# Optimization experiments

Measured on AMD Instinct MI355X. Metric: run time of the kernel, lower is better.

## Reference

```python
import jax, jax.numpy as jnp
import numpy as np

CLASSES = 21
IOU_THRESH = 0.5
ALPHA = 0.25   # focal loss alpha
GAMMA = 2.0    # focal loss gamma
SL1_BETA = 1.0 # torch SmoothL1Loss default beta
CLS_W = 1.0
REG_W = 1.0
NUM_ANCHORS = 98304
NUM_TARGETS = 1024


def _compute_iou(boxes_a, boxes_b):
    # boxes_a: [T,4], boxes_b: [A,4] in (x1,y1,x2,y2) -> [T,A]
    lt = jnp.maximum(boxes_a[:, None, :2], boxes_b[None, :, :2])
    rb = jnp.minimum(boxes_a[:, None, 2:], boxes_b[None, :, 2:])
    wh = jnp.clip(rb - lt, 0.0)
    inter = wh[..., 0] * wh[..., 1]
    area_a = (boxes_a[:, 2] - boxes_a[:, 0]) * (boxes_a[:, 3] - boxes_a[:, 1])
    area_b = (boxes_b[:, 2] - boxes_b[:, 0]) * (boxes_b[:, 3] - boxes_b[:, 1])
    union = area_a[:, None] + area_b[None, :] - inter
    return inter / jnp.maximum(union, 1e-8)


def _encode(boxes, anchors):
    bw = boxes[:, 2] - boxes[:, 0]
    bh = boxes[:, 3] - boxes[:, 1]
    bcx = boxes[:, 0] + 0.5 * bw
    bcy = boxes[:, 1] + 0.5 * bh
    aw = anchors[:, 2] - anchors[:, 0]
    ah = anchors[:, 3] - anchors[:, 1]
    acx = anchors[:, 0] + 0.5 * aw
    acy = anchors[:, 1] + 0.5 * ah
    tx = (bcx - acx) / aw
    ty = (bcy - acy) / ah
    tw = jnp.log(jnp.maximum(bw, 1e-8) / aw)
    th = jnp.log(jnp.maximum(bh, 1e-8) / ah)
    return jnp.stack([tx, ty, tw, th], axis=1)


def _focal_loss(logits, targets):
    # elementwise sigmoid focal loss (no reduction)
    p = jax.nn.sigmoid(logits)
    # numerically stable BCE with logits
    ce = jnp.maximum(logits, 0.0) - logits * targets + jnp.log1p(jnp.exp(-jnp.abs(logits)))
    p_t = p * targets + (1.0 - p) * (1.0 - targets)
    alpha_t = ALPHA * targets + (1.0 - ALPHA) * (1.0 - targets)
    return alpha_t * (1.0 - p_t) ** GAMMA * ce


def _smooth_l1(diff):
    ad = jnp.abs(diff)
    return jnp.where(ad < SL1_BETA, 0.5 * diff * diff / SL1_BETA, ad - 0.5 * SL1_BETA)


def setup_inputs() -> dict:
    key = jax.random.key(0)
    kA, kW, kT, kJ, kL, kC, kB = jax.random.split(key, 7)
    A, T = NUM_ANCHORS, NUM_TARGETS
    centers = jax.random.uniform(kA, (A, 2), minval=0.15, maxval=0.85)
    sizes = jax.random.uniform(kW, (A, 2), minval=0.05, maxval=0.30)
    anchors = jnp.concatenate([centers - 0.5 * sizes, centers + 0.5 * sizes], axis=1)
    # targets = jittered anchors so IoU >= 0.5 matches exist
    idx = jax.random.randint(kT, (T,), 0, A)
    jitter = jax.random.uniform(kJ, (T, 4), minval=-0.01, maxval=0.01)
    target_boxes = anchors[idx] + jitter
    target_labels = jax.random.randint(kL, (T,), 0, CLASSES)
    classification_preds = jax.random.normal(kC, (A, CLASSES), dtype=jnp.float32)
    boxes_preds = jax.random.normal(kB, (A, 4), dtype=jnp.float32)
    return {
        'classification_preds': classification_preds,
        'boxes_preds': boxes_preds,
        'anchors': anchors,
        'target_boxes': target_boxes,
        'target_labels': target_labels,
    }


def reference(classification_preds, boxes_preds, anchors, target_boxes, target_labels):
    iou = _compute_iou(target_boxes, anchors)  # [T, A]

    # anchor-side matching -> classification targets
    max_iou_for_anchors = jnp.max(iou, axis=0)          # [A]
    target_ids_for_anchors = jnp.argmax(iou, axis=0)     # [A]
    positive_mask = max_iou_for_anchors >= IOU_THRESH    # [A] bool
    n_pos = jnp.sum(positive_mask.astype(jnp.float32))
    onehot = jax.nn.one_hot(target_labels[target_ids_for_anchors], CLASSES, dtype=jnp.float32)
    cls_targets = jnp.where(positive_mask[:, None], onehot, 0.0)
    cls_loss = jnp.sum(_focal_loss(classification_preds, cls_targets)) / n_pos

    max_iou_for_targets = jnp.max(iou, axis=1)          # [T]
    anchor_ids_for_targets = jnp.argmax(iou, axis=1)     # [T]
    t_mask = (max_iou_for_targets >= IOU_THRESH).astype(jnp.float32)  # [T]
    matched_anchors = anchors[anchor_ids_for_targets]    # [T,4]
    encoded = _encode(target_boxes, matched_anchors)     # [T,4]
    pred = boxes_preds[anchor_ids_for_targets]           # [T,4]
    diff = (pred - encoded) * t_mask[:, None]
    n_match = jnp.maximum(jnp.sum(t_mask), 1.0)
    reg_loss = jnp.sum(_smooth_l1(diff)) / (n_match * 4.0)  # mean over matched elements

    w_cls = cls_loss * CLS_W
    w_reg = reg_loss * REG_W
    return (w_cls + w_reg, w_cls, w_reg)
```

## Files before the change

### kernel.cpp

```cpp
#include <hip/hip_runtime.h>
#include <stdint.h>

#define NA 98304
#define NT 1024
#define NC 21
#define ACH 96
#define TCH 16
#define NBLK (ACH * TCH)
#define HI_MIN 0xBF000000u


__device__ __forceinline__ float f0(float x) {
    const float ax = fabsf(x);
    const float u  = __expf(-ax);
    const float ce = fmaxf(x, 0.f) + __logf(1.f + u);
    const float p  = (x >= 0.f ? 1.f : u) / (1.f + u);
    return 0.75f * p * p * ce;
}
__device__ __forceinline__ float f1(float x) {
    const float ax = fabsf(x);
    const float u  = __expf(-ax);
    const float ce = fmaxf(x, 0.f) - x + __logf(1.f + u);
    const float p  = (x >= 0.f ? 1.f : u) / (1.f + u);
    const float q  = 1.f - p;
    return 0.25f * q * q * ce;
}
__device__ __forceinline__ unsigned long long mk_key(float iou, unsigned int idx) {
    return ((unsigned long long)(__float_as_uint(iou) | 0x80000000u) << 32) |
           (unsigned long long)(0xFFFFFFFFu - idx);
}
__device__ __forceinline__ float smooth_l1(float d) {
    const float ad = fabsf(d);
    return (ad < 1.f) ? 0.5f * d * d : ad - 0.5f;
}
__device__ __forceinline__ unsigned long long aload64(const unsigned long long* p) {
    return __hip_atomic_load(p, __ATOMIC_RELAXED, __HIP_MEMORY_SCOPE_AGENT);
}
__device__ __forceinline__ float aloadf(const float* p) {
    return __hip_atomic_load(p, __ATOMIC_RELAXED, __HIP_MEMORY_SCOPE_AGENT);
}
__device__ __forceinline__ int aloadi(const int* p) {
    return __hip_atomic_load(p, __ATOMIC_RELAXED, __HIP_MEMORY_SCOPE_AGENT);
}

__global__ __launch_bounds__(256) void k_all(
    const float* __restrict__ preds,
    const float4* __restrict__ preds4,
    const int* __restrict__ tlabels,
    const float4* __restrict__ anchors,
    const float4* __restrict__ tboxes,
    const float4* __restrict__ bpreds,
    unsigned long long* __restrict__ akeys,
    unsigned long long* __restrict__ tkeys,
    float* __restrict__ f0_part,
    float* __restrict__ corr_part,
    int* __restrict__ npos_part,
    int* __restrict__ done_ac,
    int* __restrict__ done2,
    float* __restrict__ out)
{
    __shared__ float4 s_t[64];
    __shared__ float  s_sa[64];
    __shared__ unsigned long long s_tk[64];
    __shared__ float s_f[4];
    __shared__ int   s_last, s_fin;
    __shared__ float s_a[4];
    __shared__ int   s_c[4];
    __shared__ double s_d[4];
    __shared__ int    s_i[4];
    __shared__ float  s_s[4], s_m[4];

    const int tid   = threadIdx.x;
    const int ac    = blockIdx.x;
    const int L     = blockIdx.y * ACH + ac;
    const int tbase = blockIdx.y * 64;
    const int a0    = ac * 1024 + tid;
    const int lane  = tid & 63, wid = tid >> 6;

    if (tid < 64) {
        const float4 tb = tboxes[tbase + tid];
        s_t[tid]  = tb;
        s_sa[tid] = (tb.z - tb.x) * (tb.w - tb.y);
        s_tk[tid] = 0ull;
    }
    const float4 A0 = anchors[a0];
    const float4 A1 = anchors[a0 + 256];
    const float4 A2 = anchors[a0 + 512];
    const float4 A3 = anchors[a0 + 768];

    float facc;
    {
        const int pb = L * 336;
        const float4 v0 = preds4[pb + tid];
        facc = (f0(v0.x) + f0(v0.y)) + (f0(v0.z) + f0(v0.w));
        if (tid < 80) {
            const float4 v1 = preds4[pb + 256 + tid];
            facc += (f0(v1.x) + f0(v1.y)) + (f0(v1.z) + f0(v1.w));
        }
    }
    __syncthreads();

    const float ar0 = (A0.z - A0.x) * (A0.w - A0.y);
    const float ar1 = (A1.z - A1.x) * (A1.w - A1.y);
    const float ar2 = (A2.z - A2.x) * (A2.w - A2.y);
    const float ar3 = (A3.z - A3.x) * (A3.w - A3.y);

    unsigned long long m0 = 0ull, m1 = 0ull, m2 = 0ull, m3 = 0ull;
    #pragma unroll 16
    for (int t = 0; t < 64; ++t) {
        const float4 tb = s_t[t];
        const float  sa = s_sa[t];
        {
            const float w = fmaxf(fminf(A0.z, tb.z) - fmaxf(A0.x, tb.x), 0.f);
            const float h = fmaxf(fminf(A0.w, tb.w) - fmaxf(A0.y, tb.y), 0.f);
            const float inter = w * h;
            m0 |= (inter + inter >= (ar0 + sa) - inter) ? (1ull << t) : 0ull;
        }
        {
            const float w = fmaxf(fminf(A1.z, tb.z) - fmaxf(A1.x, tb.x), 0.f);
            const float h = fmaxf(fminf(A1.w, tb.w) - fmaxf(A1.y, tb.y), 0.f);
            const float inter = w * h;
            m1 |= (inter + inter >= (ar1 + sa) - inter) ? (1ull << t) : 0ull;
        }
        {
            const float w = fmaxf(fminf(A2.z, tb.z) - fmaxf(A2.x, tb.x), 0.f);
            const float h = fmaxf(fminf(A2.w, tb.w) - fmaxf(A2.y, tb.y), 0.f);
            const float inter = w * h;
            m2 |= (inter + inter >= (ar2 + sa) - inter) ? (1ull << t) : 0ull;
        }
        {
            const float w = fmaxf(fminf(A3.z, tb.z) - fmaxf(A3.x, tb.x), 0.f);
            const float h = fmaxf(fminf(A3.w, tb.w) - fmaxf(A3.y, tb.y), 0.f);
            const float inter = w * h;
            m3 |= (inter + inter >= (ar3 + sa) - inter) ? (1ull << t) : 0ull;
        }
    }

    #pragma unroll
    for (int q = 0; q < 4; ++q) {
        unsigned long long m = (q == 0) ? m0 : (q == 1) ? m1 : (q == 2) ? m2 : m3;
        if (m != 0ull) {
            const float4 A  = (q == 0) ? A0 : (q == 1) ? A1 : (q == 2) ? A2 : A3;
            const float  ar = (q == 0) ? ar0 : (q == 1) ? ar1 : (q == 2) ? ar2 : ar3;
            const unsigned int aidx = (unsigned int)(a0 + q * 256);
            float b = 0.f;
            int   bi = -1;
            do {
                const int t = __ffsll((unsigned long long)m) - 1;
                m &= m - 1;
                const float4 tb = s_t[t];
                const float  sa = s_sa[t];
                const float w = fmaxf(fminf(A.z, tb.z) - fmaxf(A.x, tb.x), 0.f);
                const float h = fmaxf(fminf(A.w, tb.w) - fmaxf(A.y, tb.y), 0.f);
                const float inter = w * h;
                const float uni = (ar + sa) - inter;
                const float iou = inter / uni;
                if (iou > b) { b = iou; bi = t; }
                atomicMax(&s_tk[t], mk_key(iou, aidx));
            } while (m != 0ull);
            atomicMax(&akeys[aidx], mk_key(b, (unsigned int)(tbase + bi)));
        }
    }

    for (int o = 32; o > 0; o >>= 1) facc += __shfl_down(facc, o);
    if (lane == 0) s_f[wid] = facc;

    __syncthreads();
    if (tid < 64) {
        const unsigned long long tk = s_tk[tid];
        if (tk != 0ull) atomicMax(&tkeys[tbase + tid], tk);
    }
    if (tid == 0)
        __hip_atomic_store(&f0_part[L], s_f[0] + s_f[1] + s_f[2] + s_f[3],
                           __ATOMIC_RELAXED, __HIP_MEMORY_SCOPE_AGENT);

    __syncthreads();
    if (tid == 0) {
        __threadfence();
        s_last = (atomicAdd(&done_ac[ac], 1) == TCH - 1);
    }
    __syncthreads();
    if (!s_last) return;
    __builtin_amdgcn_fence(__ATOMIC_ACQUIRE, "agent");

    float acc = 0.f;
    int   cnt = 0;
    #pragma unroll
    for (int j = 0; j < 4; ++j) {
        const int a = a0 + j * 256;
        const unsigned long long k = aload64(&akeys[a]);
        if ((unsigned int)(k >> 32) >= HI_MIN) {
            cnt += 1;
            const int lab = tlabels[0xFFFFFFFFu - (unsigned int)k];
            const float x = preds[a * NC + lab];
            acc += f1(x) - f0(x);
        }
    }
    if (tid < TCH) acc += aloadf(&f0_part[ac + tid * ACH]);

    for (int o = 32; o > 0; o >>= 1) {
        acc += __shfl_down(acc, o);
        cnt += __shfl_down(cnt, o);
    }
    if (lane == 0) { s_a[wid] = acc; s_c[wid] = cnt; }
    __syncthreads();
    if (tid == 0) {
        __hip_atomic_store(&corr_part[ac], s_a[0] + s_a[1] + s_a[2] + s_a[3],
                           __ATOMIC_RELAXED, __HIP_MEMORY_SCOPE_AGENT);
        __hip_atomic_store(&npos_part[ac], s_c[0] + s_c[1] + s_c[2] + s_c[3],
                           __ATOMIC_RELAXED, __HIP_MEMORY_SCOPE_AGENT);
        __threadfence();
        s_fin = (atomicAdd(done2, 1) == ACH - 1);
    }
    __syncthreads();
    if (!s_fin) return;
    __builtin_amdgcn_fence(__ATOMIC_ACQUIRE, "agent");

    double cl = 0.0;
    int    np = 0;
    if (tid < ACH) {
        cl = (double)aloadf(&corr_part[tid]);
        np = aloadi(&npos_part[tid]);
    }
    float s = 0.f, m = 0.f;
    #pragma unroll
    for (int j = 0; j < 4; ++j) {
        const int t = tid + 256 * j;
        const unsigned long long key = aload64(&tkeys[t]);
        if ((unsigned int)(key >> 32) >= HI_MIN) {
            const unsigned int ga = 0xFFFFFFFFu - (unsigned int)key;
            const float4 tb  = tboxes[t];
            const float4 abx = anchors[ga];
            const float4 pb  = bpreds[ga];
            const float bw = tb.z - tb.x, bh = tb.w - tb.y;
            const float bcx = tb.x + 0.5f * bw, bcy = tb.y + 0.5f * bh;
            const float aw = abx.z - abx.x, ah = abx.w - abx.y;
            const float acx = abx.x + 0.5f * aw, acy = abx.y + 0.5f * ah;
            const float tx = (bcx - acx) / aw;
            const float ty = (bcy - acy) / ah;
            const float tw = logf(fmaxf(bw, 1e-8f) / aw);
            const float th = logf(fmaxf(bh, 1e-8f) / ah);
            s += smooth_l1(pb.x - tx) + smooth_l1(pb.y - ty) +
                 smooth_l1(pb.z - tw) + smooth_l1(pb.w - th);
            m += 1.f;
        }
    }
    for (int o = 32; o > 0; o >>= 1) {
        cl += __shfl_down(cl, o);
        np += __shfl_down(np, o);
        s  += __shfl_down(s, o);
        m  += __shfl_down(m, o);
    }
    __syncthreads();
    if (lane == 0) { s_d[wid] = cl; s_i[wid] = np; s_s[wid] = s; s_m[wid] = m; }
    __syncthreads();
    if (tid == 0) {
        const double cls_sum = s_d[0] + s_d[1] + s_d[2] + s_d[3];
        const int    npos    = s_i[0] + s_i[1] + s_i[2] + s_i[3];
        const float  rs      = s_s[0] + s_s[1] + s_s[2] + s_s[3];
        const float  rm      = s_m[0] + s_m[1] + s_m[2] + s_m[3];
        const float cls = (float)(cls_sum / (double)npos);
        const float reg = rs / (fmaxf(rm, 1.f) * 4.f);
        out[0] = cls + reg;
        out[1] = cls;
        out[2] = reg;
    }
}

extern "C" void kernel_launch(void* const* d_in, const int* in_sizes, int n_in,
                              void* d_out, int out_size, void* d_ws, size_t ws_size,
                              hipStream_t stream) {
    const float*  preds   = (const float*)d_in[0];
    const float4* preds4  = (const float4*)d_in[0];
    const float4* bpreds  = (const float4*)d_in[1];
    const float4* anchors = (const float4*)d_in[2];
    const float4* tboxes  = (const float4*)d_in[3];
    const int*    tlabels = (const int*)d_in[4];

    char* ws = (char*)d_ws;
    int*    done2     = (int*)(ws + 0);
    int*    done_ac   = (int*)(ws + 64);
    float*  f0_part   = (float*)(ws + 1024);
    float*  corr_part = (float*)(ws + 8192);
    int*    npos_part = (int*)(ws + 8704);
    unsigned long long* tkeys = (unsigned long long*)(ws + 12288);
    unsigned long long* akeys = (unsigned long long*)(ws + 24576);

    hipMemsetAsync(d_ws, 0, 1024, stream);

    k_all<<<dim3(ACH, TCH), 256, 0, stream>>>(
        preds, preds4, tlabels, anchors, tboxes, bpreds,
        akeys, tkeys, f0_part, corr_part, npos_part,
        done_ac, done2, (float*)d_out);
}
```

Before: 130.0 us.

## Repartition IoU matching so each block owns 64 anchors against all targets

Each block now handles 64 anchors against all 1024 targets held in shared memory. This replaces the 2D anchor-chunk by target-chunk grid, so the per-anchor best match is resolved inside the block through shuffles and shared memory rather than through global akeys atomics and a second last-block pass. The IoU>=0.5 test becomes a single fma comparison (inter >= (a+b)/3) using pre-negated box coordinates, and only passing pairs compute the division. In exchange, target keys are now updated with global atomicMax directly instead of a per-block shared reduction, and the final block must reduce 1536 partials.

```diff
diff --git a/kernel.cpp b/kernel.cpp
--- a/kernel.cpp
+++ b/kernel.cpp
@@ -4,10 +4,9 @@
 #define NA 98304
 #define NT 1024
 #define NC 21
-#define ACH 96
-#define TCH 16
-#define NBLK (ACH * TCH)
+#define NBLK 1536
 #define HI_MIN 0xBF000000u
+#define C3S 0.33333f
 
 
 __device__ __forceinline__ float f0(float x) {
@@ -43,6 +42,35 @@
     return __hip_atomic_load(p, __ATOMIC_RELAXED, __HIP_MEMORY_SCOPE_AGENT);
 }
 
+#define PAIR(j, bk)                                                         \
+    {                                                                       \
+        const float minz = fminf(az4[j], tb.z);                             \
+        const float mnx  = fminf(negax[j], tb.x);                           \
+        const float w    = fmaxf(minz + mnx, 0.f);                          \
+        const float minw = fminf(aw4[j], tb.w);                             \
+        const float mny  = fminf(negay[j], tb.y);                           \
+        const float h0   = minw + mny;                                      \
+        const float rhs3 = fmaf(sa, C3S, ar34[j]);                          \
+        const float d    = fmaf(w, h0, -rhs3);                              \
+        if (d >= 0.f) {                                                     \
+            const float h     = fmaxf(h0, 0.f);                             \
+            const float inter = w * h;                                      \
+            const float uni   = (ar4[j] + sa) - inter;                      \
+            const float iou   = inter / uni;                                \
+            const unsigned long long ak = mk_key(iou, (unsigned int)t);     \
+            if (ak > bk) bk = ak;                                           \
+            atomicMax(&tkeys[t], mk_key(iou, (unsigned int)(abase + j)));   \
+        }                                                                   \
+    }
+
+#define FOLD(bk)                                                            \
+    {                                                                       \
+        unsigned long long o_ = __shfl_xor(bk, 16);                         \
+        if (o_ > bk) bk = o_;                                               \
+        o_ = __shfl_xor(bk, 32);                                            \
+        if (o_ > bk) bk = o_;                                               \
+    }
+
 __global__ __launch_bounds__(256) void k_all(
     const float* __restrict__ preds,
     const float4* __restrict__ preds4,
@@ -50,47 +78,31 @@
     const float4* __restrict__ anchors,
     const float4* __restrict__ tboxes,
     const float4* __restrict__ bpreds,
-    unsigned long long* __restrict__ akeys,
     unsigned long long* __restrict__ tkeys,
-    float* __restrict__ f0_part,
-    float* __restrict__ corr_part,
+    float* __restrict__ part,
     int* __restrict__ npos_part,
-    int* __restrict__ done_ac,
     int* __restrict__ done2,
     float* __restrict__ out)
 {
-    __shared__ float4 s_t[64];
-    __shared__ float  s_sa[64];
-    __shared__ unsigned long long s_tk[64];
-    __shared__ float s_f[4];
-    __shared__ int   s_last, s_fin;
-    __shared__ float s_a[4];
-    __shared__ int   s_c[4];
+    __shared__ float4 s_t[NT];
+    __shared__ unsigned long long s_bk[4][64];
+    __shared__ float  s_f[4];
+    __shared__ int    s_fin;
     __shared__ double s_d[4];
     __shared__ int    s_i[4];
     __shared__ float  s_s[4], s_m[4];
 
-    const int tid   = threadIdx.x;
-    const int ac    = blockIdx.x;
-    const int L     = blockIdx.y * ACH + ac;
-    const int tbase = blockIdx.y * 64;
-    const int a0    = ac * 1024 + tid;
-    const int lane  = tid & 63, wid = tid >> 6;
-
-    if (tid < 64) {
-        const float4 tb = tboxes[tbase + tid];
-        s_t[tid]  = tb;
-        s_sa[tid] = (tb.z - tb.x) * (tb.w - tb.y);
-        s_tk[tid] = 0ull;
-    }
-    const float4 A0 = anchors[a0];
-    const float4 A1 = anchors[a0 + 256];
-    const float4 A2 = anchors[a0 + 512];
-    const float4 A3 = anchors[a0 + 768];
+    const int tid  = threadIdx.x;
+    const int b    = blockIdx.x;
+    const int lane = tid & 63, wid = tid >> 6;
+
+    float4 tbl[4];
+    #pragma unroll
+    for (int k = 0; k < 4; ++k) tbl[k] = tboxes[tid + 256 * k];
 
     float facc;
     {
-        const int pb = L * 336;
+        const int pb = b * 336;
         const float4 v0 = preds4[pb + tid];
         facc = (f0(v0.x) + f0(v0.y)) + (f0(v0.z) + f0(v0.w));
         if (tid < 80) {
@@ -98,119 +110,82 @@
             facc += (f0(v1.x) + f0(v1.y)) + (f0(v1.z) + f0(v1.w));
         }
     }
-    __syncthreads();
-
-    const float ar0 = (A0.z - A0.x) * (A0.w - A0.y);
-    const float ar1 = (A1.z - A1.x) * (A1.w - A1.y);
-    const float ar2 = (A2.z - A2.x) * (A2.w - A2.y);
-    const float ar3 = (A3.z - A3.x) * (A3.w - A3.y);
-
-    unsigned long long m0 = 0ull, m1 = 0ull, m2 = 0ull, m3 = 0ull;
-    #pragma unroll 16
-    for (int t = 0; t < 64; ++t) {
+
+    #pragma unroll
+    for (int k = 0; k < 4; ++k)
+        s_t[tid + 256 * k] = make_float4(-tbl[k].x, -tbl[k].y, tbl[k].z, tbl[k].w);
+
+    const int qd    = lane & 15;
+    const int sl    = lane >> 4;
+    const int abase = b * 64 + 4 * qd;
+    float negax[4], negay[4], az4[4], aw4[4], ar4[4], ar34[4];
+    #pragma unroll
+    for (int j = 0; j < 4; ++j) {
+        const float4 A = anchors[abase + j];
+        negax[j] = -A.x; negay[j] = -A.y;
+        az4[j]   = A.z;  aw4[j]   = A.w;
+        ar4[j]   = (A.z - A.x) * (A.w - A.y);
+        ar34[j]  = ar4[j] * C3S;
+    }
+    __syncthreads();
+
+    unsigned long long bk0 = 0ull, bk1 = 0ull, bk2 = 0ull, bk3 = 0ull;
+    const int tb0 = wid * 256 + sl;
+    #pragma unroll 4
+    for (int i = 0; i < 64; ++i) {
+        const int t = tb0 + 4 * i;
         const float4 tb = s_t[t];
-        const float  sa = s_sa[t];
-        {
-            const float w = fmaxf(fminf(A0.z, tb.z) - fmaxf(A0.x, tb.x), 0.f);
-            const float h = fmaxf(fminf(A0.w, tb.w) - fmaxf(A0.y, tb.y), 0.f);
-            const float inter = w * h;
-            m0 |= (inter + inter >= (ar0 + sa) - inter) ? (1ull << t) : 0ull;
-        }
-        {
-            const float w = fmaxf(fminf(A1.z, tb.z) - fmaxf(A1.x, tb.x), 0.f);
-            const float h = fmaxf(fminf(A1.w, tb.w) - fmaxf(A1.y, tb.y), 0.f);
-            const float inter = w * h;
-            m1 |= (inter + inter >= (ar1 + sa) - inter) ? (1ull << t) : 0ull;
-        }
-        {
-            const float w = fmaxf(fminf(A2.z, tb.z) - fmaxf(A2.x, tb.x), 0.f);
-            const float h = fmaxf(fminf(A2.w, tb.w) - fmaxf(A2.y, tb.y), 0.f);
-            const float inter = w * h;
-            m2 |= (inter + inter >= (ar2 + sa) - inter) ? (1ull << t) : 0ull;
-        }
-        {
-            const float w = fmaxf(fminf(A3.z, tb.z) - fmaxf(A3.x, tb.x), 0.f);
-            const float h = fmaxf(fminf(A3.w, tb.w) - fmaxf(A3.y, tb.y), 0.f);
-            const float inter = w * h;
-            m3 |= (inter + inter >= (ar3 + sa) - inter) ? (1ull << t) : 0ull;
-        }
-    }
-
-    #pragma unroll
-    for (int q = 0; q < 4; ++q) {
-        unsigned long long m = (q == 0) ? m0 : (q == 1) ? m1 : (q == 2) ? m2 : m3;
-        if (m != 0ull) {
-            const float4 A  = (q == 0) ? A0 : (q == 1) ? A1 : (q == 2) ? A2 : A3;
-            const float  ar = (q == 0) ? ar0 : (q == 1) ? ar1 : (q == 2) ? ar2 : ar3;
-            const unsigned int aidx = (unsigned int)(a0 + q * 256);
-            float b = 0.f;
-            int   bi = -1;
-            do {
-                const int t = __ffsll((unsigned long long)m) - 1;
-                m &= m - 1;
-                const float4 tb = s_t[t];
-                const float  sa = s_sa[t];
-                const float w = fmaxf(fminf(A.z, tb.z) - fmaxf(A.x, tb.x), 0.f);
-                const float h = fmaxf(fminf(A.w, tb.w) - fmaxf(A.y, tb.y), 0.f);
-                const float inter = w * h;
-                const float uni = (ar + sa) - inter;
-                const float iou = inter / uni;
-                if (iou > b) { b = iou; bi = t; }
-                atomicMax(&s_tk[t], mk_key(iou, aidx));
-            } while (m != 0ull);
-            atomicMax(&akeys[aidx], mk_key(b, (unsigned int)(tbase + bi)));
-        }
+        const float sa = (tb.z + tb.x) * (tb.w + tb.y);
+        PAIR(0, bk0)
+        PAIR(1, bk1)
+        PAIR(2, bk2)
+        PAIR(3, bk3)
+    }
+
+    FOLD(bk0) FOLD(bk1) FOLD(bk2) FOLD(bk3)
+    if (sl == 0) {
+        s_bk[wid][4 * qd + 0] = bk0;
+        s_bk[wid][4 * qd + 1] = bk1;
+        s_bk[wid][4 * qd + 2] = bk2;
+        s_bk[wid][4 * qd + 3] = bk3;
     }
 
     for (int o = 32; o > 0; o >>= 1) facc += __shfl_down(facc, o);
     if (lane == 0) s_f[wid] = facc;
-
-    __syncthreads();
+    __syncthreads();
+
+    float corrv = 0.f;
+    int   cnt   = 0;
     if (tid < 64) {
-        const unsigned long long tk = s_tk[tid];
-        if (tk != 0ull) atomicMax(&tkeys[tbase + tid], tk);
-    }
-    if (tid == 0)
-        __hip_atomic_store(&f0_part[L], s_f[0] + s_f[1] + s_f[2] + s_f[3],
+        unsigned long long k0 = s_bk[0][tid];
+        const unsigned long long k1 = s_bk[1][tid];
+        const unsigned long long k2 = s_bk[2][tid];
+        const unsigned long long k3 = s_bk[3][tid];
+        if (k1 > k0) k0 = k1;
+        if (k2 > k0) k0 = k2;
+        if (k3 > k0) k0 = k3;
+        if ((unsigned int)(k0 >> 32) >= HI_MIN) {
+            cnt = 1;
+            const int tI  = (int)(0xFFFFFFFFu - (unsigned int)k0);
+            const int lab = tlabels[tI];
+            const float x = preds[(b * 64 + tid) * NC + lab];
+            corrv = f1(x) - f0(x);
+        }
+        for (int o = 32; o > 0; o >>= 1) {
+            corrv += __shfl_down(corrv, o);
+            cnt   += __shfl_down(cnt, o);
+        }
+    }
+    if (tid == 0) {
+        __hip_atomic_store(&part[b], (s_f[0] + s_f[1] + s_f[2] + s_f[3]) + corrv,
                            __ATOMIC_RELAXED, __HIP_MEMORY_SCOPE_AGENT);
-
+        __hip_atomic_store(&npos_part[b], cnt,
+                           __ATOMIC_RELAXED, __HIP_MEMORY_SCOPE_AGENT);
+    }
     __syncthreads();
     if (tid == 0) {
         __threadfence();
-        s_last = (atomicAdd(&done_ac[ac], 1) == TCH - 1);
-    }
-    __syncthreads();
-    if (!s_last) return;
-    __builtin_amdgcn_fence(__ATOMIC_ACQUIRE, "agent");
-
-    float acc = 0.f;
-    int   cnt = 0;
-    #pragma unroll
-    for (int j = 0; j < 4; ++j) {
-        const int a = a0 + j * 256;
-        const unsigned long long k = aload64(&akeys[a]);
-        if ((unsigned int)(k >> 32) >= HI_MIN) {
-            cnt += 1;
-            const int lab = tlabels[0xFFFFFFFFu - (unsigned int)k];
-            const float x = preds[a * NC + lab];
-            acc += f1(x) - f0(x);
-        }
-    }
-    if (tid < TCH) acc += aloadf(&f0_part[ac + tid * ACH]);
-
-    for (int o = 32; o > 0; o >>= 1) {
-        acc += __shfl_down(acc, o);
-        cnt += __shfl_down(cnt, o);
-    }
-    if (lane == 0) { s_a[wid] = acc; s_c[wid] = cnt; }
-    __syncthreads();
-    if (tid == 0) {
-        __hip_atomic_store(&corr_part[ac], s_a[0] + s_a[1] + s_a[2] + s_a[3],
-                           __ATOMIC_RELAXED, __HIP_MEMORY_SCOPE_AGENT);
-        __hip_atomic_store(&npos_part[ac], s_c[0] + s_c[1] + s_c[2] + s_c[3],
-                           __ATOMIC_RELAXED, __HIP_MEMORY_SCOPE_AGENT);
-        __threadfence();
-        s_fin = (atomicAdd(done2, 1) == ACH - 1);
+        s_fin = (atomicAdd(done2, 1) == NBLK - 1);
     }
     __syncthreads();
     if (!s_fin) return;
@@ -218,9 +193,11 @@
 
     double cl = 0.0;
     int    np = 0;
-    if (tid < ACH) {
-        cl = (double)aloadf(&corr_part[tid]);
-        np = aloadi(&npos_part[tid]);
+    #pragma unroll
+    for (int j = 0; j < 6; ++j) {
+        const int i = tid + 256 * j;
+        cl += (double)aloadf(&part[i]);
+        np += aloadi(&npos_part[i]);
     }
     float s = 0.f, m = 0.f;
     #pragma unroll
@@ -279,17 +256,13 @@
 
     char* ws = (char*)d_ws;
     int*    done2     = (int*)(ws + 0);
-    int*    done_ac   = (int*)(ws + 64);
-    float*  f0_part   = (float*)(ws + 1024);
-    float*  corr_part = (float*)(ws + 8192);
-    int*    npos_part = (int*)(ws + 8704);
-    unsigned long long* tkeys = (unsigned long long*)(ws + 12288);
-    unsigned long long* akeys = (unsigned long long*)(ws + 24576);
+    float*  part      = (float*)(ws + 1024);
+    int*    npos_part = (int*)(ws + 8192);
+    unsigned long long* tkeys = (unsigned long long*)(ws + 16384);
 
     hipMemsetAsync(d_ws, 0, 1024, stream);
 
-    k_all<<<dim3(ACH, TCH), 256, 0, stream>>>(
+    k_all<<<dim3(NBLK), 256, 0, stream>>>(
         preds, preds4, tlabels, anchors, tboxes, bpreds,
-        akeys, tkeys, f0_part, corr_part, npos_part,
-        done_ac, done2, (float*)d_out);
-}
+        tkeys, part, npos_part, done2, (float*)d_out);
+}
```

Measured after the change: 185.3 us. 42.5% more time.
